# Performance work log

Hardware: AMD Instinct MI355X
Metric: run time of the kernel (lower is better)

The kernel has to match this reference:

```python
import jax, jax.numpy as jnp
import numpy as np


def _ln(x, g, eps=1e-5):
    # channel LayerNorm over dim 1, unbiased=False variance
    mean = jnp.mean(x, axis=1, keepdims=True)
    var = jnp.mean((x - mean) ** 2, axis=1, keepdims=True)
    return (x - mean) * jax.lax.rsqrt(var + eps) * g


def _c11(x, w, b):
    # 1x1 conv: w (O,C), b (O,)
    return jnp.einsum('bchw,oc->bohw', x, w) + b[None, :, None, None]


def _dw(x, w, b):
    # depthwise 3x3 conv, SAME padding; w (C,1,3,3), b (C,)
    C = x.shape[1]
    y = jax.lax.conv_general_dilated(x, w, (1, 1), 'SAME',
                                     feature_group_count=C,
                                     dimension_numbers=('NCHW', 'OIHW', 'NCHW'))
    return y + b[None, :, None, None]


def _forward(F_i, F_w, g1, g2, qw1, qb1, kw1, kb1, vw1, vb1,
             qw2, qb2, kw2, kb2, vw2, vb2,
             qdw1, qdb1, kdw1, kdb1, vdw1, vdb1,
             qdw2, qdb2, kdw2, kdb2, vdw2, vdb2, lw, lb):
    B, C1, H, W = F_i.shape
    C2 = F_w.shape[1]
    HW = H * W
    fi = _ln(F_i, g1)
    fw = _ln(F_w, g2)
    # qkv = 1x1 conv -> depthwise conv; then RAW C-order reshape (torch .view)
    Qi = _dw(_c11(fi, qw1, qb1), qdw1, qdb1).reshape(B, HW, C1)
    Ki = _dw(_c11(fi, kw1, kb1), kdw1, kdb1).reshape(B, HW, C1)
    Vi = _dw(_c11(fi, vw1, vb1), vdw1, vdb1).reshape(B, C1, HW)
    Qw = _dw(_c11(fw, qw2, qb2), qdw2, qdb2).reshape(B, HW, C2)
    Kw = _dw(_c11(fw, kw2, kb2), kdw2, kdb2).reshape(B, HW, C2)
    Vw = _dw(_c11(fw, vw2, vb2), vdw2, vdb2).reshape(B, C2, HW)
    # channel cross-attention: (B,C1,HW)@(B,HW,C2) -> (B,C1,C2)
    a1 = jax.nn.softmax(jnp.einsum('bnc,bnd->bcd', Qi, Kw), axis=-1)
    a2 = jax.nn.softmax(jnp.einsum('bnc,bnd->bcd', Qw, Ki), axis=-1)
    Aw = jnp.einsum('bcd,bdn->bcn', a1, Vw).reshape(B, H, W, C2).transpose(0, 3, 1, 2)
    Ai = jnp.einsum('bcd,bdn->bcn', a2, Vi).reshape(B, H, W, C1).transpose(0, 3, 1, 2)
    cat = jnp.concatenate([Aw, Ai], axis=1)  # (B, C2+C1, H, W)
    Ct = cat.shape[1]
    flat = cat.reshape(B, Ct, HW).transpose(0, 2, 1).reshape(-1, Ct)  # (B*HW, Ct)
    out = flat @ lw.T + lb  # (B*HW, Cout)
    Cout = lb.shape[0]
    # faithful replication of torch's view/permute/view tail
    out = out.reshape(B, Cout, H, W).transpose(0, 2, 3, 1).reshape(B, Cout, H, W)
    return out + F_i + F_w


def setup_inputs() -> dict:
    key = jax.random.key(0)
    ks = jax.random.split(key, 20)
    B, C, H, W = 8, 128, 128, 128
    d = {}
    d['F_i'] = jax.random.normal(ks[0], (B, C, H, W), jnp.float32)
    d['F_w'] = jax.random.normal(ks[1], (B, C, H, W), jnp.float32)
    d['g1'] = jnp.ones((1, C, 1, 1), jnp.float32)
    d['g2'] = jnp.ones((1, C, 1, 1), jnp.float32)
    s = 1.0 / np.sqrt(C)
    i = 2
    for n in ['qw1', 'kw1', 'vw1', 'qw2', 'kw2', 'vw2']:
        d[n] = jax.random.normal(ks[i], (C, C), jnp.float32) * s
        i += 1
    for n in ['qb1', 'kb1', 'vb1', 'qb2', 'kb2', 'vb2']:
        d[n] = jnp.zeros((C,), jnp.float32)
    sd = 1.0 / 3.0
    for n in ['qdw1', 'kdw1', 'vdw1', 'qdw2', 'kdw2', 'vdw2']:
        d[n] = jax.random.normal(ks[i], (C, 1, 3, 3), jnp.float32) * sd
        i += 1
    for n in ['qdb1', 'kdb1', 'vdb1', 'qdb2', 'kdb2', 'vdb2']:
        d[n] = jnp.zeros((C,), jnp.float32)
    d['lw'] = jax.random.normal(ks[i], (C, 2 * C), jnp.float32) * (1.0 / np.sqrt(2 * C))
    d['lb'] = jnp.zeros((C,), jnp.float32)
    return d


def reference(F_i, F_w, g1, g2, qw1, qb1, kw1, kb1, vw1, vb1,
              qw2, qb2, kw2, kb2, vw2, vb2,
              qdw1, qdb1, kdw1, kdb1, vdw1, vdb1,
              qdw2, qdb2, kdw2, kdb2, vdw2, vdb2, lw, lb):
    return _forward(F_i, F_w, g1, g2, qw1, qb1, kw1, kb1, vw1, vb1,
                    qw2, qb2, kw2, kb2, vw2, vb2,
                    qdw1, qdb1, kdw1, kdb1, vdw1, vdb1,
                    qdw2, qdb2, kdw2, kdb2, vdw2, vdb2, lw, lb)
```

## Files before the change

### kernel.cpp

```cpp
#include <hip/hip_runtime.h>
#include <cstddef>
#include <cstring>

#define HW 16384
#define CC 128
#define NB 8
#define GB 4

typedef short bf16x8_t __attribute__((ext_vector_type(8)));
typedef float floatx4 __attribute__((ext_vector_type(4)));

__device__ inline unsigned short f2bf(float f) {
  unsigned u; __builtin_memcpy(&u, &f, 4);
  u += 0x7fffu + ((u >> 16) & 1u);
  return (unsigned short)(u >> 16);
}
__device__ inline float bf2f(unsigned short s) {
  unsigned u = ((unsigned)s) << 16; float f; __builtin_memcpy(&f, &u, 4);
  return f;
}

__global__ __launch_bounds__(256) void k_prep_w(
    const float* __restrict__ qw1, const float* __restrict__ kw1,
    const float* __restrict__ vw1, const float* __restrict__ qw2,
    const float* __restrict__ kw2, const float* __restrict__ vw2,
    const float* __restrict__ g1, const float* __restrict__ g2,
    const float* __restrict__ lw,
    unsigned short* __restrict__ Wsplit, unsigned short* __restrict__ lwbf) {
  const int t = threadIdx.x;
  const int m = blockIdx.y;
  if (m < 6) {
    const float* W = (m == 0) ? qw1 : (m == 1) ? kw1 : (m == 2) ? vw1
                   : (m == 3) ? qw2 : (m == 4) ? kw2 : vw2;
    const float* g = (m < 3) ? g1 : g2;
    const int idx = blockIdx.x * 256 + t;
    const int o = idx >> 4;
    const int c0 = (idx & 15) * 8;
    unsigned short* hi = Wsplit + m * 32768 + o * 128 + c0;
    unsigned short* lo = hi + 16384;
#pragma unroll
    for (int j = 0; j < 8; ++j) {
      float v = W[o * 128 + c0 + j] * g[c0 + j];
      unsigned short h = f2bf(v);
      hi[j] = h;
      lo[j] = f2bf(v - bf2f(h));
    }
  } else {
    const int idx = blockIdx.x * 256 + t;
#pragma unroll
    for (int j = 0; j < 16; ++j)
      lwbf[idx * 16 + j] = f2bf(lw[idx * 16 + j]);
  }
}

__global__ __launch_bounds__(256) void k_ln_stats(const float* __restrict__ x,
                                                  float* __restrict__ mean,
                                                  float* __restrict__ rstd) {
  int idx = blockIdx.x * 256 + threadIdx.x;
  int p2 = idx * 2;
  int b = p2 >> 14;
  int p = p2 & (HW - 1);
  const float* xp = x + ((size_t)b << 21) + p;
  float s0 = 0.f, ss0 = 0.f, s1 = 0.f, ss1 = 0.f;
  for (int c = 0; c < CC; ++c) {
    float2 v = *reinterpret_cast<const float2*>(xp + ((size_t)c << 14));
    s0 += v.x; ss0 += v.x * v.x;
    s1 += v.y; ss1 += v.y * v.y;
  }
  float m0 = s0 * (1.0f / CC), m1 = s1 * (1.0f / CC);
  float var0 = ss0 * (1.0f / CC) - m0 * m0;
  float var1 = ss1 * (1.0f / CC) - m1 * m1;
  *reinterpret_cast<float2*>(mean + p2) = (float2){m0, m1};
  *reinterpret_cast<float2*>(rstd + p2) =
      (float2){rsqrtf(var0 + 1e-5f), rsqrtf(var1 + 1e-5f)};
}

__global__ __launch_bounds__(256, 4) void k_conv1x1_mfma(
    const float* __restrict__ X,
    const unsigned short* __restrict__ Whi, const unsigned short* __restrict__ Wlo,
    const float* __restrict__ bias,
    const float* __restrict__ mean, const float* __restrict__ rstd,
    float* __restrict__ Y, int b0) {
  const int bl = blockIdx.y;
  const int b = b0 + bl;
  const int p0 = blockIdx.x * 64;
  const int t = threadIdx.x;
  const int lane = t & 63, wv = t >> 6;
  const int quad = lane >> 4, l15 = lane & 15;
  const int wr = wv >> 1, wc = wv & 1;

  const float* Xb = X + ((size_t)b << 21);
  int pj[2]; float muj[2], rsj[2];
#pragma unroll
  for (int j = 0; j < 2; ++j) {
    pj[j] = p0 + wc * 32 + j * 16 + l15;
    muj[j] = mean[b * HW + pj[j]];
    rsj[j] = rstd[b * HW + pj[j]];
  }

  floatx4 acc[4][2];
#pragma unroll
  for (int i = 0; i < 4; ++i)
#pragma unroll
    for (int j = 0; j < 2; ++j) acc[i][j] = (floatx4){0.f, 0.f, 0.f, 0.f};

  for (int k0 = 0; k0 < 128; k0 += 32) {
    bf16x8_t afh[4], afl[4];
#pragma unroll
    for (int i = 0; i < 4; ++i) {
      const int m = wr * 64 + i * 16 + l15;
      afh[i] = *reinterpret_cast<const bf16x8_t*>(Whi + m * 128 + k0 + quad * 8);
      afl[i] = *reinterpret_cast<const bf16x8_t*>(Wlo + m * 128 + k0 + quad * 8);
    }
    float xv[2][8];
#pragma unroll
    for (int j = 0; j < 2; ++j) {
      const float* xp = Xb + ((size_t)(k0 + quad * 8) << 14) + pj[j];
#pragma unroll
      for (int jj = 0; jj < 8; ++jj)
        xv[j][jj] = xp[(size_t)jj << 14];
    }
    bf16x8_t bfh[2], bfl[2];
#pragma unroll
    for (int j = 0; j < 2; ++j) {
      short th[8], tl[8];
#pragma unroll
      for (int jj = 0; jj < 8; ++jj) {
        float v = (xv[j][jj] - muj[j]) * rsj[j];
        unsigned short h = f2bf(v);
        th[jj] = (short)h;
        tl[jj] = (short)f2bf(v - bf2f(h));
      }
      bfh[j] = *reinterpret_cast<bf16x8_t*>(&th[0]);
      bfl[j] = *reinterpret_cast<bf16x8_t*>(&tl[0]);
    }
#pragma unroll
    for (int i = 0; i < 4; ++i)
#pragma unroll
      for (int j = 0; j < 2; ++j) {
        acc[i][j] = __builtin_amdgcn_mfma_f32_16x16x32_bf16(afh[i], bfh[j], acc[i][j], 0, 0, 0);
        acc[i][j] = __builtin_amdgcn_mfma_f32_16x16x32_bf16(afh[i], bfl[j], acc[i][j], 0, 0, 0);
        acc[i][j] = __builtin_amdgcn_mfma_f32_16x16x32_bf16(afl[i], bfh[j], acc[i][j], 0, 0, 0);
      }
  }
  float* Yb = Y + ((size_t)bl << 21);
#pragma unroll
  for (int i = 0; i < 4; ++i) {
#pragma unroll
    for (int j = 0; j < 2; ++j) {
#pragma unroll
      for (int r = 0; r < 4; ++r) {
        const int o = wr * 64 + i * 16 + quad * 4 + r;
        const int p = p0 + wc * 32 + j * 16 + l15;
        Yb[((size_t)o << 14) + p] = acc[i][j][r] + bias[o];
      }
    }
  }
}

__global__ __launch_bounds__(256) void k_score_mfma(
    const float* __restrict__ Yq, const float* __restrict__ Yk,
    const float* __restrict__ qdw, const float* __restrict__ qdb,
    const float* __restrict__ kdw, const float* __restrict__ kdb,
    float* __restrict__ P) {
  __shared__ __align__(16) float raw[32][132];
  __shared__ __align__(16) short Ah[128][40];
  __shared__ __align__(16) short Al[128][40];
  __shared__ __align__(16) short Bh[128][40];
  __shared__ __align__(16) short Bl[128][40];
  const int ch = blockIdx.x;
  const int bl = blockIdx.y;
  const int t = threadIdx.x;
  const int lane = t & 63, wv = t >> 6;
  const int quad = lane >> 4, l15 = lane & 15;
  const int wr = wv >> 1, wc = wv & 1;
  const int h_loc = t >> 3;
  const int w0 = (t & 7) * 16;
  const int s2w = t & 127, s2o = t >> 7;
  const int cc = ch;
  const float* Yqb = Yq + ((size_t)bl << 21) + ((size_t)cc << 14);
  const float* Ykb = Yk + ((size_t)bl << 21) + ((size_t)cc << 14);
  const float* qwt = qdw + cc * 9;
  const float* kwt = kdw + cc * 9;
  const float qbv = qdb[cc], kbv = kdb[cc];

  floatx4 acc[4][4];
#pragma unroll
  for (int i = 0; i < 4; ++i)
#pragma unroll
    for (int j = 0; j < 4; ++j) acc[i][j] = (floatx4){0.f, 0.f, 0.f, 0.f};

  for (int k0 = 0; k0 < 128; k0 += 32) {
    const int h = k0 + h_loc;
#pragma unroll
    for (int side = 0; side < 2; ++side) {
      const float* Yc = side ? Ykb : Yqb;
      const float* wt = side ? kwt : qwt;
      const float bias = side ? kbv : qbv;
      float a[16];
#pragma unroll
      for (int j = 0; j < 16; ++j) a[j] = bias;
#pragma unroll
      for (int dy = 0; dy < 3; ++dy) {
        const int hh = h + dy - 1;
        if (hh < 0 || hh > 127) continue;
        const float* rp = Yc + (hh << 7) + w0;
        float4 f0 = *reinterpret_cast<const float4*>(rp);
        float4 f1 = *reinterpret_cast<const float4*>(rp + 4);
        float4 f2 = *reinterpret_cast<const float4*>(rp + 8);
        float4 f3 = *reinterpret_cast<const float4*>(rp + 12);
        float s[18];
        s[1] = f0.x;  s[2] = f0.y;  s[3] = f0.z;  s[4] = f0.w;
        s[5] = f1.x;  s[6] = f1.y;  s[7] = f1.z;  s[8] = f1.w;
        s[9] = f2.x;  s[10] = f2.y; s[11] = f2.z; s[12] = f2.w;
        s[13] = f3.x; s[14] = f3.y; s[15] = f3.z; s[16] = f3.w;
        s[0] = (w0 > 0) ? rp[-1] : 0.f;
        s[17] = (w0 < 112) ? rp[16] : 0.f;
        const float wa = wt[dy * 3 + 0], wb = wt[dy * 3 + 1], wc2 = wt[dy * 3 + 2];
#pragma unroll
        for (int j = 0; j < 16; ++j)
          a[j] = fmaf(s[j], wa, fmaf(s[j + 1], wb, fmaf(s[j + 2], wc2, a[j])));
      }
#pragma unroll
      for (int u = 0; u < 4; ++u)
        *reinterpret_cast<float4*>(&raw[h_loc][w0 + 4 * u]) =
            (float4){a[4 * u], a[4 * u + 1], a[4 * u + 2], a[4 * u + 3]};
      __syncthreads();
      short* dh = side ? &Bh[0][0] : &Ah[0][0];
      short* dl = side ? &Bl[0][0] : &Al[0][0];
#pragma unroll
      for (int item = 0; item < 2; ++item) {
        const int oct = s2o + 2 * item;
        short th[8], tl[8];
#pragma unroll
        for (int jj = 0; jj < 8; ++jj) {
          float v = raw[oct * 8 + jj][s2w];
          unsigned short hb = f2bf(v);
          th[jj] = (short)hb;
          tl[jj] = (short)f2bf(v - bf2f(hb));
        }
        *reinterpret_cast<bf16x8_t*>(&dh[s2w * 40 + oct * 8]) =
            *reinterpret_cast<bf16x8_t*>(&th[0]);
        *reinterpret_cast<bf16x8_t*>(&dl[s2w * 40 + oct * 8]) =
            *reinterpret_cast<bf16x8_t*>(&tl[0]);
      }
      __syncthreads();
    }
    bf16x8_t afh[4], afl[4], bfh[4], bfl[4];
#pragma unroll
    for (int i = 0; i < 4; ++i) {
      const int m = wr * 64 + i * 16 + l15;
      afh[i] = *reinterpret_cast<const bf16x8_t*>(&Ah[m][quad * 8]);
      afl[i] = *reinterpret_cast<const bf16x8_t*>(&Al[m][quad * 8]);
    }
#pragma unroll
    for (int j = 0; j < 4; ++j) {
      const int n = wc * 64 + j * 16 + l15;
      bfh[j] = *reinterpret_cast<const bf16x8_t*>(&Bh[n][quad * 8]);
      bfl[j] = *reinterpret_cast<const bf16x8_t*>(&Bl[n][quad * 8]);
    }
#pragma unroll
    for (int i = 0; i < 4; ++i)
#pragma unroll
      for (int j = 0; j < 4; ++j) {
        acc[i][j] = __builtin_amdgcn_mfma_f32_16x16x32_bf16(afh[i], bfh[j], acc[i][j], 0, 0, 0);
        acc[i][j] = __builtin_amdgcn_mfma_f32_16x16x32_bf16(afh[i], bfl[j], acc[i][j], 0, 0, 0);
        acc[i][j] = __builtin_amdgcn_mfma_f32_16x16x32_bf16(afl[i], bfh[j], acc[i][j], 0, 0, 0);
      }
  }
  float* Pp = P + ((size_t)(ch * GB + bl) << 14);
#pragma unroll
  for (int i = 0; i < 4; ++i) {
#pragma unroll
    for (int j = 0; j < 4; ++j) {
#pragma unroll
      for (int r = 0; r < 4; ++r) {
        const int c = wr * 64 + i * 16 + quad * 4 + r;
        const int d = wc * 64 + j * 16 + l15;
        Pp[c * 128 + d] = acc[i][j][r];
      }
    }
  }
}

__global__ __launch_bounds__(128) void k_reduce_softmax(
    const float* __restrict__ P, unsigned short* __restrict__ Sbf) {
  __shared__ float red[128];
  const int row = blockIdx.x;
  const int bl = row >> 7, c = row & 127;
  const int t = threadIdx.x;
  const size_t rem = ((size_t)c << 7) + t;
  float v = 0.f;
  for (int ch = 0; ch < 128; ++ch)
    v += P[((size_t)(ch * GB + bl) << 14) + rem];
  red[t] = v;
  __syncthreads();
  for (int s = 64; s > 0; s >>= 1) {
    if (t < s) red[t] = fmaxf(red[t], red[t + s]);
    __syncthreads();
  }
  float mx = red[0];
  __syncthreads();
  float e = expf(v - mx);
  red[t] = e;
  __syncthreads();
  for (int s = 64; s > 0; s >>= 1) {
    if (t < s) red[t] += red[t + s];
    __syncthreads();
  }
  Sbf[((size_t)bl << 14) + rem] = f2bf(e / red[0]);
}

__global__ __launch_bounds__(256) void k_dw_t(const float* __restrict__ Y,
                                              const float* __restrict__ Kw,
                                              const float* __restrict__ db,
                                              unsigned short* __restrict__ Vt) {
  __shared__ unsigned short T[128][33];
  const int h = blockIdx.x;
  const int c0 = blockIdx.y * 32;
  const int bl = blockIdx.z;
  const int t = threadIdx.x;
  const int cl = t >> 3;
  const int w0 = (t & 7) * 16;
  const int c = c0 + cl;
  const float* Yc = Y + ((size_t)bl << 21) + ((size_t)c << 14);
  const float* wt = Kw + c * 9;
  float a[16];
#pragma unroll
  for (int j = 0; j < 16; ++j) a[j] = db[c];
#pragma unroll
  for (int dy = 0; dy < 3; ++dy) {
    const int hh = h + dy - 1;
    if (hh < 0 || hh > 127) continue;
    const float* rp = Yc + (hh << 7) + w0;
    float4 f0 = *reinterpret_cast<const float4*>(rp);
    float4 f1 = *reinterpret_cast<const float4*>(rp + 4);
    float4 f2 = *reinterpret_cast<const float4*>(rp + 8);
    float4 f3 = *reinterpret_cast<const float4*>(rp + 12);
    float s[18];
    s[1] = f0.x;  s[2] = f0.y;  s[3] = f0.z;  s[4] = f0.w;
    s[5] = f1.x;  s[6] = f1.y;  s[7] = f1.z;  s[8] = f1.w;
    s[9] = f2.x;  s[10] = f2.y; s[11] = f2.z; s[12] = f2.w;
    s[13] = f3.x; s[14] = f3.y; s[15] = f3.z; s[16] = f3.w;
    s[0] = (w0 > 0) ? rp[-1] : 0.f;
    s[17] = (w0 < 112) ? rp[16] : 0.f;
    const float wa = wt[dy * 3 + 0], wb = wt[dy * 3 + 1], wc2 = wt[dy * 3 + 2];
#pragma unroll
    for (int j = 0; j < 16; ++j)
      a[j] = fmaf(s[j], wa, fmaf(s[j + 1], wb, fmaf(s[j + 2], wc2, a[j])));
  }
#pragma unroll
  for (int j = 0; j < 16; ++j) T[w0 + j][cl] = f2bf(a[j]);
  __syncthreads();
  const int w = t >> 1, half = t & 1;
  unsigned short tmp[16];
#pragma unroll
  for (int j = 0; j < 16; ++j) tmp[j] = T[w][half * 16 + j];
  uint4 v0, v1;
  unsigned* vp0 = reinterpret_cast<unsigned*>(&v0);
  unsigned* vp1 = reinterpret_cast<unsigned*>(&v1);
#pragma unroll
  for (int j = 0; j < 4; ++j) {
    vp0[j] = (unsigned)tmp[2 * j] | ((unsigned)tmp[2 * j + 1] << 16);
    vp1[j] = (unsigned)tmp[8 + 2 * j] | ((unsigned)tmp[8 + 2 * j + 1] << 16);
  }
  unsigned short* dst = Vt + ((size_t)bl << 21) + ((size_t)((h << 7) + w) << 7)
                        + c0 + half * 16;
  *reinterpret_cast<uint4*>(dst) = v0;
  *reinterpret_cast<uint4*>(dst + 8) = v1;
}

__global__ __launch_bounds__(256) void k_av_mfma(
    const unsigned short* __restrict__ Sbf, const unsigned short* __restrict__ Vt,
    unsigned short* __restrict__ O) {
  const int bl = blockIdx.y;
  const int p0 = blockIdx.x * 128;
  const int t = threadIdx.x;
  const int lane = t & 63, wv = t >> 6;
  const int quad = lane >> 4, l15 = lane & 15;
  const int wr = wv >> 1, wc = wv & 1;
  const unsigned short* Sb = Sbf + ((size_t)bl << 14);
  floatx4 acc[4][4];
#pragma unroll
  for (int i = 0; i < 4; ++i)
#pragma unroll
    for (int j = 0; j < 4; ++j) acc[i][j] = (floatx4){0.f, 0.f, 0.f, 0.f};
  const unsigned short* Vb = Vt + ((size_t)bl << 21);
#pragma unroll
  for (int d0 = 0; d0 < 128; d0 += 32) {
    bf16x8_t af[4], bf[4];
#pragma unroll
    for (int i = 0; i < 4; ++i) {
      const int m = wr * 64 + i * 16 + l15;
      af[i] = *reinterpret_cast<const bf16x8_t*>(Sb + m * 128 + d0 + quad * 8);
    }
#pragma unroll
    for (int j = 0; j < 4; ++j) {
      const int p = p0 + wc * 64 + j * 16 + l15;
      bf[j] = *reinterpret_cast<const bf16x8_t*>(Vb + ((size_t)p << 7) + d0 + quad * 8);
    }
#pragma unroll
    for (int i = 0; i < 4; ++i)
#pragma unroll
      for (int j = 0; j < 4; ++j)
        acc[i][j] = __builtin_amdgcn_mfma_f32_16x16x32_bf16(af[i], bf[j], acc[i][j], 0, 0, 0);
  }
  unsigned short* Ob = O + ((size_t)bl << 21);
#pragma unroll
  for (int i = 0; i < 4; ++i) {
#pragma unroll
    for (int j = 0; j < 4; ++j) {
#pragma unroll
      for (int r = 0; r < 4; ++r) {
        const int c = wr * 64 + i * 16 + quad * 4 + r;
        const int p = p0 + wc * 64 + j * 16 + l15;
        Ob[((size_t)c << 14) + p] = f2bf(acc[i][j][r]);
      }
    }
  }
}

__global__ __launch_bounds__(256) void k_final2_mfma(
    const unsigned short* __restrict__ A1, const unsigned short* __restrict__ A2,
    const unsigned short* __restrict__ lwbf, const float* __restrict__ lb,
    const float* __restrict__ Fi, const float* __restrict__ Fw,
    float* __restrict__ out, int b0) {
  const int c2 = blockIdx.x;
  const int bl = blockIdx.y;
  const int b = b0 + bl;
  const int t = threadIdx.x;
  const int lane = t & 63, wv = t >> 6;
  const int quad = lane >> 4, l15 = lane & 15;
  const int wr = wv >> 1, wc = wv & 1;
  floatx4 acc[4][4];
#pragma unroll
  for (int i = 0; i < 4; ++i)
#pragma unroll
    for (int j = 0; j < 4; ++j) acc[i][j] = (floatx4){0.f, 0.f, 0.f, 0.f};
#pragma unroll
  for (int phase = 0; phase < 2; ++phase) {
    const unsigned short* Ub = (phase ? A2 : A1) + ((size_t)bl << 21) + c2 * 128;
#pragma unroll
    for (int d0 = 0; d0 < 128; d0 += 32) {
      bf16x8_t af[4], bf[4];
#pragma unroll
      for (int i = 0; i < 4; ++i) {
        const int m = wr * 64 + i * 16 + l15;
        af[i] = *reinterpret_cast<const bf16x8_t*>(
            lwbf + m * 256 + phase * 128 + d0 + quad * 8);
      }
#pragma unroll
      for (int j = 0; j < 4; ++j) {
        const int n = wc * 64 + j * 16 + l15;
        bf[j] = *reinterpret_cast<const bf16x8_t*>(Ub + ((size_t)n << 14) + d0 + quad * 8);
      }
#pragma unroll
      for (int i = 0; i < 4; ++i)
#pragma unroll
        for (int j = 0; j < 4; ++j)
          acc[i][j] = __builtin_amdgcn_mfma_f32_16x16x32_bf16(af[i], bf[j], acc[i][j], 0, 0, 0);
    }
  }
  const size_t obase = ((size_t)b << 21) + ((size_t)c2 << 14);
#pragma unroll
  for (int i = 0; i < 4; ++i) {
#pragma unroll
    for (int j = 0; j < 4; ++j) {
#pragma unroll
      for (int r = 0; r < 4; ++r) {
        const int h2 = wr * 64 + i * 16 + quad * 4 + r;
        const int w2 = wc * 64 + j * 16 + l15;
        const size_t a = obase + ((size_t)h2 << 7) + w2;
        out[a] = acc[i][j][r] + lb[h2] + Fi[a] + Fw[a];
      }
    }
  }
}

extern "C" void kernel_launch(void* const* d_in, const int* in_sizes, int n_in,
                              void* d_out, int out_size, void* d_ws, size_t ws_size,
                              hipStream_t stream) {
  const float* F_i  = (const float*)d_in[0];
  const float* F_w  = (const float*)d_in[1];
  const float* g1   = (const float*)d_in[2];
  const float* g2   = (const float*)d_in[3];
  const float* qw1  = (const float*)d_in[4];
  const float* kw1  = (const float*)d_in[5];
  const float* vw1  = (const float*)d_in[6];
  const float* qw2  = (const float*)d_in[7];
  const float* kw2  = (const float*)d_in[8];
  const float* vw2  = (const float*)d_in[9];
  const float* qb1  = (const float*)d_in[10];
  const float* kb1  = (const float*)d_in[11];
  const float* vb1  = (const float*)d_in[12];
  const float* qb2  = (const float*)d_in[13];
  const float* kb2  = (const float*)d_in[14];
  const float* vb2  = (const float*)d_in[15];
  const float* qdw1 = (const float*)d_in[16];
  const float* kdw1 = (const float*)d_in[17];
  const float* vdw1 = (const float*)d_in[18];
  const float* qdw2 = (const float*)d_in[19];
  const float* kdw2 = (const float*)d_in[20];
  const float* vdw2 = (const float*)d_in[21];
  const float* qdb1 = (const float*)d_in[22];
  const float* kdb1 = (const float*)d_in[23];
  const float* vdb1 = (const float*)d_in[24];
  const float* qdb2 = (const float*)d_in[25];
  const float* kdb2 = (const float*)d_in[26];
  const float* vdb2 = (const float*)d_in[27];
  const float* lw   = (const float*)d_in[28];
  const float* lb   = (const float*)d_in[29];
  float* out = (float*)d_out;

  char* w = (char*)d_ws;
  const size_t NTOT = (size_t)NB * HW;
  float* meanI = (float*)w; w += NTOT * 4;
  float* rstdI = (float*)w; w += NTOT * 4;
  float* meanW = (float*)w; w += NTOT * 4;
  float* rstdW = (float*)w; w += NTOT * 4;
  unsigned short* Sbf = (unsigned short*)w; w += (size_t)GB * HW * 2;
  unsigned short* Wsplit = (unsigned short*)w; w += 6 * 32768 * 2;
  unsigned short* lwbf = (unsigned short*)w; w += 32768 * 2;
  float* P     = (float*)w; w += (size_t)128 * GB * HW * 4;
  float* Yq    = (float*)w; w += ((size_t)GB << 21) * 4;
  char*  Ykreg = w;         w += ((size_t)GB << 21) * 4;
  float* Yk    = (float*)Ykreg;
  unsigned short* Vt = (unsigned short*)Ykreg;
  unsigned short* A2 = (unsigned short*)(Ykreg + ((size_t)GB << 21) * 2);
  unsigned short* A1 = (unsigned short*)w; w += ((size_t)GB << 21) * 2;

  const unsigned short* Wh0 = Wsplit + 0 * 32768;
  const unsigned short* Wh1 = Wsplit + 1 * 32768;
  const unsigned short* Wh2 = Wsplit + 2 * 32768;
  const unsigned short* Wh3 = Wsplit + 3 * 32768;
  const unsigned short* Wh4 = Wsplit + 4 * 32768;
  const unsigned short* Wh5 = Wsplit + 5 * 32768;

  dim3 blk(256);
  k_prep_w<<<dim3(8, 7), blk, 0, stream>>>(qw1, kw1, vw1, qw2, kw2, vw2,
                                           g1, g2, lw, Wsplit, lwbf);
  k_ln_stats<<<dim3(256), blk, 0, stream>>>(F_i, meanI, rstdI);
  k_ln_stats<<<dim3(256), blk, 0, stream>>>(F_w, meanW, rstdW);

  for (int b0 = 0; b0 < NB; b0 += GB) {
    k_conv1x1_mfma<<<dim3(256, GB), blk, 0, stream>>>(F_i, Wh0, Wh0 + 16384, qb1, meanI, rstdI, Yq, b0);
    k_conv1x1_mfma<<<dim3(256, GB), blk, 0, stream>>>(F_w, Wh4, Wh4 + 16384, kb2, meanW, rstdW, Yk, b0);
    k_score_mfma<<<dim3(128, GB), blk, 0, stream>>>(Yq, Yk, qdw1, qdb1, kdw2, kdb2, P);
    k_reduce_softmax<<<dim3(GB * 128), dim3(128), 0, stream>>>(P, Sbf);
    k_conv1x1_mfma<<<dim3(256, GB), blk, 0, stream>>>(F_w, Wh5, Wh5 + 16384, vb2, meanW, rstdW, Yq, b0);
    k_dw_t<<<dim3(128, 4, GB), blk, 0, stream>>>(Yq, vdw2, vdb2, Vt);
    k_av_mfma<<<dim3(128, GB), blk, 0, stream>>>(Sbf, Vt, A1);

    k_conv1x1_mfma<<<dim3(256, GB), blk, 0, stream>>>(F_w, Wh3, Wh3 + 16384, qb2, meanW, rstdW, Yq, b0);
    k_conv1x1_mfma<<<dim3(256, GB), blk, 0, stream>>>(F_i, Wh1, Wh1 + 16384, kb1, meanI, rstdI, Yk, b0);
    k_score_mfma<<<dim3(128, GB), blk, 0, stream>>>(Yq, Yk, qdw2, qdb2, kdw1, kdb1, P);
    k_reduce_softmax<<<dim3(GB * 128), dim3(128), 0, stream>>>(P, Sbf);
    k_conv1x1_mfma<<<dim3(256, GB), blk, 0, stream>>>(F_i, Wh2, Wh2 + 16384, vb1, meanI, rstdI, Yq, b0);
    k_dw_t<<<dim3(128, 4, GB), blk, 0, stream>>>(Yq, vdw1, vdb1, Vt);
    k_av_mfma<<<dim3(128, GB), blk, 0, stream>>>(Sbf, Vt, A2);

    k_final2_mfma<<<dim3(128, GB), blk, 0, stream>>>(A1, A2, lwbf, lb, F_i, F_w, out, b0);
  }
}
```

Baseline: 875.1 us.

## Stage activation tile through LDS in 1x1 conv and convert once per element

The 1x1 conv kernel now loads each 32x64 activation tile with coalesced float4 reads into shared memory, normalizes and splits it into bf16 hi/lo once per element, and writes the fragments to LDS for the MFMA operands to read. Previously each wave re-read and re-converted the same activations with strided scalar global loads, so the two row-waves duplicated the work. The change adds three barriers per k-step and LDS usage, and drops the occupancy hint from the launch bounds.

After: 862.4 us. No clear change (-1.4%).

```diff
diff --git a/kernel.cpp b/kernel.cpp
--- a/kernel.cpp
+++ b/kernel.cpp
@@ -75,12 +75,15 @@
       (float2){rsqrtf(var0 + 1e-5f), rsqrtf(var1 + 1e-5f)};
 }
 
-__global__ __launch_bounds__(256, 4) void k_conv1x1_mfma(
+__global__ __launch_bounds__(256) void k_conv1x1_mfma(
     const float* __restrict__ X,
     const unsigned short* __restrict__ Whi, const unsigned short* __restrict__ Wlo,
     const float* __restrict__ bias,
     const float* __restrict__ mean, const float* __restrict__ rstd,
     float* __restrict__ Y, int b0) {
+  __shared__ __align__(16) float raw[32][68];
+  __shared__ __align__(16) short Bh[64][40];
+  __shared__ __align__(16) short Bl[64][40];
   const int bl = blockIdx.y;
   const int b = b0 + bl;
   const int p0 = blockIdx.x * 64;
@@ -89,15 +92,12 @@
   const int quad = lane >> 4, l15 = lane & 15;
   const int wr = wv >> 1, wc = wv & 1;
 
+  const int s1c = t >> 3, s1p = (t & 7) * 8;
+  const int s2p = t & 63, s2o = t >> 6;
+  const float mu = mean[b * HW + p0 + s2p];
+  const float rs = rstd[b * HW + p0 + s2p];
+
   const float* Xb = X + ((size_t)b << 21);
-  int pj[2]; float muj[2], rsj[2];
-#pragma unroll
-  for (int j = 0; j < 2; ++j) {
-    pj[j] = p0 + wc * 32 + j * 16 + l15;
-    muj[j] = mean[b * HW + pj[j]];
-    rsj[j] = rstd[b * HW + pj[j]];
-  }
-
   floatx4 acc[4][2];
 #pragma unroll
   for (int i = 0; i < 4; ++i)
@@ -105,34 +105,41 @@
     for (int j = 0; j < 2; ++j) acc[i][j] = (floatx4){0.f, 0.f, 0.f, 0.f};
 
   for (int k0 = 0; k0 < 128; k0 += 32) {
-    bf16x8_t afh[4], afl[4];
+    {
+      const float* xp = Xb + ((size_t)(k0 + s1c) << 14) + p0 + s1p;
+      *reinterpret_cast<float4*>(&raw[s1c][s1p]) =
+          *reinterpret_cast<const float4*>(xp);
+      *reinterpret_cast<float4*>(&raw[s1c][s1p + 4]) =
+          *reinterpret_cast<const float4*>(xp + 4);
+    }
+    __syncthreads();
+    {
+      short th[8], tl[8];
+#pragma unroll
+      for (int jj = 0; jj < 8; ++jj) {
+        float v = (raw[s2o * 8 + jj][s2p] - mu) * rs;
+        unsigned short h = f2bf(v);
+        th[jj] = (short)h;
+        tl[jj] = (short)f2bf(v - bf2f(h));
+      }
+      *reinterpret_cast<bf16x8_t*>(&Bh[s2p][s2o * 8]) =
+          *reinterpret_cast<bf16x8_t*>(&th[0]);
+      *reinterpret_cast<bf16x8_t*>(&Bl[s2p][s2o * 8]) =
+          *reinterpret_cast<bf16x8_t*>(&tl[0]);
+    }
+    __syncthreads();
+    bf16x8_t afh[4], afl[4], bfh[2], bfl[2];
 #pragma unroll
     for (int i = 0; i < 4; ++i) {
       const int m = wr * 64 + i * 16 + l15;
       afh[i] = *reinterpret_cast<const bf16x8_t*>(Whi + m * 128 + k0 + quad * 8);
       afl[i] = *reinterpret_cast<const bf16x8_t*>(Wlo + m * 128 + k0 + quad * 8);
     }
-    float xv[2][8];
 #pragma unroll
     for (int j = 0; j < 2; ++j) {
-      const float* xp = Xb + ((size_t)(k0 + quad * 8) << 14) + pj[j];
-#pragma unroll
-      for (int jj = 0; jj < 8; ++jj)
-        xv[j][jj] = xp[(size_t)jj << 14];
-    }
-    bf16x8_t bfh[2], bfl[2];
-#pragma unroll
-    for (int j = 0; j < 2; ++j) {
-      short th[8], tl[8];
-#pragma unroll
-      for (int jj = 0; jj < 8; ++jj) {
-        float v = (xv[j][jj] - muj[j]) * rsj[j];
-        unsigned short h = f2bf(v);
-        th[jj] = (short)h;
-        tl[jj] = (short)f2bf(v - bf2f(h));
-      }
-      bfh[j] = *reinterpret_cast<bf16x8_t*>(&th[0]);
-      bfl[j] = *reinterpret_cast<bf16x8_t*>(&tl[0]);
+      const int p = wc * 32 + j * 16 + l15;
+      bfh[j] = *reinterpret_cast<const bf16x8_t*>(&Bh[p][quad * 8]);
+      bfl[j] = *reinterpret_cast<const bf16x8_t*>(&Bl[p][quad * 8]);
     }
 #pragma unroll
     for (int i = 0; i < 4; ++i)
@@ -142,6 +149,7 @@
         acc[i][j] = __builtin_amdgcn_mfma_f32_16x16x32_bf16(afh[i], bfl[j], acc[i][j], 0, 0, 0);
         acc[i][j] = __builtin_amdgcn_mfma_f32_16x16x32_bf16(afl[i], bfh[j], acc[i][j], 0, 0, 0);
       }
+    __syncthreads();
   }
   float* Yb = Y + ((size_t)bl << 21);
 #pragma unroll
```
